# Kernel optimization log

Measured on AMD Instinct MI355X. Metric: run time of the kernel, lower is better.

## Reference

```python
import jax, jax.numpy as jnp
import numpy as np

INPUT_SIZE = 512
SLOT_SIZE = 256
MLP_HIDDEN = 512
NUM_SLOTS = 8
NUM_ITERS = 3
EPSILON = 1e-6
LN_EPS = 1e-5


def _layernorm(x, g, b):
    m = jnp.mean(x, axis=-1, keepdims=True)
    v = jnp.mean(jnp.square(x - m), axis=-1, keepdims=True)
    return (x - m) * jax.lax.rsqrt(v + LN_EPS) * g + b


def setup_inputs() -> dict:
    key = jax.random.key(0)
    ks = jax.random.split(key, 16)
    N, B, W = 32, 64, 24
    s = 0.02
    inp = {
        "sentence": jax.random.normal(ks[0], (N, B, W, INPUT_SIZE), jnp.float32),
        "sentence_sum": jax.random.normal(ks[1], (N, B, INPUT_SIZE), jnp.float32),
        "mask": jax.random.randint(ks[2], (N, B, W), 0, 2, jnp.int32),
        "Wk": jax.random.normal(ks[3], (INPUT_SIZE, SLOT_SIZE), jnp.float32) * s,
        "bk": jnp.zeros((SLOT_SIZE,), jnp.float32),
        "Wv": jax.random.normal(ks[4], (INPUT_SIZE, SLOT_SIZE), jnp.float32) * s,
        "bv": jnp.zeros((SLOT_SIZE,), jnp.float32),
        "Wq": jax.random.normal(ks[5], (SLOT_SIZE, SLOT_SIZE), jnp.float32) * s,
        "bq": jnp.zeros((SLOT_SIZE,), jnp.float32),
        "g_ln": jnp.ones((SLOT_SIZE,), jnp.float32),
        "b_ln": jnp.zeros((SLOT_SIZE,), jnp.float32),
        "W1": jax.random.normal(ks[6], (SLOT_SIZE, MLP_HIDDEN), jnp.float32) * s,
        "b1": jnp.zeros((MLP_HIDDEN,), jnp.float32),
        "W2": jax.random.normal(ks[7], (MLP_HIDDEN, SLOT_SIZE), jnp.float32) * s,
        "b2": jnp.zeros((SLOT_SIZE,), jnp.float32),
        "Wbind": jax.random.normal(ks[8], (INPUT_SIZE, NUM_SLOTS * SLOT_SIZE), jnp.float32) * s,
        "bbind": jnp.zeros((NUM_SLOTS * SLOT_SIZE,), jnp.float32),
        "Wproj": jax.random.normal(ks[9], (2 * SLOT_SIZE, SLOT_SIZE), jnp.float32) * s,
        "bproj": jnp.zeros((SLOT_SIZE,), jnp.float32),
    }
    return inp


def reference(sentence, sentence_sum, mask, Wk, bk, Wv, bv, Wq, bq, g_ln, b_ln,
              W1, b1, W2, b2, Wbind, bbind, Wproj, bproj):
    N, B = sentence.shape[0], sentence.shape[1]
    # initial slots from the sentence summary: [N, B, NUM_SLOTS, SLOT]
    initial_slots = (sentence_sum @ Wbind + bbind).reshape(N, B, NUM_SLOTS, SLOT_SIZE)
    # additive mask on the word axis: [N, B, W, 1]
    maskf = -1e6 * (1.0 - mask.astype(jnp.float32))[..., None]
    # elu(+1) feature maps for keys; plain linear values
    k = jax.nn.elu(sentence @ Wk + bk) + 1.0  # [N,B,W,SLOT]
    v = sentence @ Wv + bv                    # [N,B,W,SLOT]

    scale = 1.0 / SLOT_SIZE
    slots = initial_slots
    for _ in range(NUM_ITERS):
        q = (slots @ Wq + bq) + initial_slots
        q = jax.nn.elu(q * (SLOT_SIZE ** -0.5)) + 1.0  # [N,B,S,SLOT]
        attn_logits = jnp.einsum('nbis,nbjs->nbij', k, q) + maskf  # [N,B,W,S]
        attn = jax.nn.softmax(attn_logits, axis=3) + EPSILON
        attn = attn / jnp.sum(attn, axis=2, keepdims=True)  # renorm over words
        updates = jnp.einsum('nbij,nbik->nbjk', attn, v)    # [N,B,S,SLOT]
        h = _layernorm(updates, g_ln, b_ln)
        h = jax.nn.relu(h @ W1 + b1) @ W2 + b2
        slots = slots + h * scale

    # dropout is identity in eval mode
    slots = jnp.concatenate([initial_slots, slots], axis=-1)
    slots = slots @ Wproj + bproj
    return slots
```

## Files before the change

kernel.cpp:

```cpp
#include <hip/hip_runtime.h>
#include <hip/hip_bf16.h>
#include <math.h>

typedef unsigned int uint;
typedef unsigned short ushort;
typedef __attribute__((ext_vector_type(8))) short bf16x8;
typedef __attribute__((ext_vector_type(4))) float f32x4;

__device__ __forceinline__ float bu2f(ushort u){ union{uint u; float f;} v; v.u = ((uint)u)<<16; return v.f; }
__device__ __forceinline__ ushort f2bu(float x){ union{float f; uint u;} v; v.f = x; uint r = (v.u + 0x7FFFu + ((v.u>>16)&1u))>>16; return (ushort)r; }
__device__ __forceinline__ uint pack2(float a, float b){ return (uint)f2bu(a) | ((uint)f2bu(b) << 16); }
__device__ __forceinline__ uint cvtpk2(float a, float b){
    uint r; asm("v_cvt_pk_bf16_f32 %0, %1, %2" : "=v"(r) : "v"(a), "v"(b)); return r;
}
__device__ __forceinline__ void gload16(const ushort* g, ushort* l){
    __builtin_amdgcn_global_load_lds(
        (const __attribute__((address_space(1))) uint*)g,
        (__attribute__((address_space(3))) uint*)l, 16, 0, 0);
}

#define GEPI_IS0   0
#define GEPI_Q     2
#define GEPI_RELU  3
#define GEPI_MLP2  4
#define GEPI_OUT   5
#define GEPI_MLP2L 6

#define SWZ(r, c) (((r) << 5) + ((((c) ^ ((r) >> 1)) & 3) << 3))


template<int EPI, int CB>
__global__ __launch_bounds__(256) void gemm64(
    const ushort* __restrict__ Abf, int lda,
    const ushort* __restrict__ Bt,
    const float* __restrict__ xb0,
    float* __restrict__ fp0,
    ushort* __restrict__ up0, ushort* __restrict__ up1,
    int M, int N, int K)
{
    __shared__ ushort As[64 * 32];
    __shared__ ushort Bs[64 * 32];
    int tid = threadIdx.x;
    int wave = tid >> 6, lane = tid & 63;
    int wr = wave >> 1, wc = wave & 1;
    int quad = lane >> 4, l15 = lane & 15;

    constexpr int LCB = (CB == 4) ? 2 : (CB == 8) ? 3 : 5;
    int bid = blockIdx.x;
    int x8  = bid & 7;
    int tt  = bid >> 3;
    int cb  = tt & (CB - 1);
    int rb  = ((tt >> LCB) << 3) + x8;
    int row0 = rb * 64, col0 = cb * 64;

    int r   = (wave << 4) + (lane >> 2);
    int csw = ((((lane & 3) ^ (r >> 1)) & 3) << 3);
    ushort* Alds = &As[wave << 9];
    ushort* Blds = &Bs[wave << 9];
    const ushort* Ag = Abf + (size_t)(row0 + r) * lda + csw;
    const ushort* Bg = Bt  + (size_t)(col0 + r) * K   + csw;

    f32x4 acc[2][2];
    #pragma unroll
    for (int i = 0; i < 2; i++)
        #pragma unroll
        for (int j = 0; j < 2; j++) acc[i][j] = (f32x4){0.f, 0.f, 0.f, 0.f};

    for (int k0 = 0; k0 < K; k0 += 32) {
        gload16(Ag + k0, Alds);
        gload16(Bg + k0, Blds);
        __syncthreads();
        bf16x8 af[2], bfr[2];
        #pragma unroll
        for (int mt = 0; mt < 2; mt++) {
            int ar = wr * 32 + mt * 16 + l15;
            af[mt] = *(const bf16x8*)&As[SWZ(ar, quad)];
        }
        #pragma unroll
        for (int nt = 0; nt < 2; nt++) {
            int br = wc * 32 + nt * 16 + l15;
            bfr[nt] = *(const bf16x8*)&Bs[SWZ(br, quad)];
        }
        #pragma unroll
        for (int mt = 0; mt < 2; mt++)
            #pragma unroll
            for (int nt = 0; nt < 2; nt++)
                acc[mt][nt] = __builtin_amdgcn_mfma_f32_16x16x32_bf16(
                    af[mt], bfr[nt], acc[mt][nt], 0, 0, 0);
        __syncthreads();
    }

    #pragma unroll
    for (int mt = 0; mt < 2; mt++) {
        #pragma unroll
        for (int nt = 0; nt < 2; nt++) {
            #pragma unroll
            for (int reg = 0; reg < 4; reg++) {
                int gr = row0 + wr * 32 + mt * 16 + quad * 4 + reg;
                int gc = col0 + wc * 32 + nt * 16 + l15;
                float x = acc[mt][nt][reg] + xb0[gc];
                if (EPI == GEPI_IS0) {
                    size_t srow = (size_t)gr * 8 + (gc >> 8);
                    int dim = gc & 255;
                    fp0[srow * 256 + dim] = x;
                    ushort xb = f2bu(x);
                    up0[srow * 512 + dim]       = xb;
                    up0[srow * 512 + 256 + dim] = xb;
                } else if (EPI == GEPI_Q) {
                    float y = (x + bu2f(up1[(size_t)gr * 512 + gc])) * 0.0625f;
                    y = y > 0.f ? y + 1.f : expf(y);
                    up0[(size_t)gr * 256 + gc] = f2bu(y);
                } else if (EPI == GEPI_RELU) {
                    up0[(size_t)gr * 512 + gc] = f2bu(fmaxf(x, 0.f));
                } else if (EPI == GEPI_MLP2 || EPI == GEPI_MLP2L) {
                    size_t i = (size_t)gr * 256 + gc;
                    float s = fp0[i] + x * (1.f / 256.f);
                    if (EPI == GEPI_MLP2) fp0[i] = s;
                    up0[(size_t)gr * 512 + 256 + gc] = f2bu(s);
                } else {
                    fp0[(size_t)gr * 256 + gc] = x;
                }
            }
        }
    }
}

__global__ __launch_bounds__(256) void gemm_kv64(
    const ushort* __restrict__ A0,
    const ushort* __restrict__ A1,
    const ushort* __restrict__ Bt,
    const float* __restrict__ bk, const float* __restrict__ bv,
    ushort* __restrict__ kbuf, ushort* __restrict__ vbuf, int K)
{
    __shared__ ushort As[64 * 32];
    __shared__ ushort Bs[64 * 32];
    int tid = threadIdx.x;
    int wave = tid >> 6, lane = tid & 63;
    int wr = wave >> 1, wc = wave & 1;
    int quad = lane >> 4, l15 = lane & 15;

    int bid = blockIdx.x;
    int x8  = bid & 7;
    int tt  = bid >> 3;
    int cb  = tt & 7;
    int rb  = (tt >> 3) * 8 + x8;
    int row0 = rb * 64, col0 = cb * 64;

    int r   = (wave << 4) + (lane >> 2);
    int csw = ((((lane & 3) ^ (r >> 1)) & 3) << 3);
    ushort* Alds = &As[wave << 9];
    ushort* Blds = &Bs[wave << 9];
    const ushort* Ag = (row0 < 32768)
        ? (A0 + (size_t)(row0 + r) * K + csw)
        : (A1 + (size_t)(row0 - 32768 + r) * K + csw);
    const ushort* Bg = Bt + (size_t)(col0 + r) * K + csw;

    f32x4 acc[2][2];
    #pragma unroll
    for (int i = 0; i < 2; i++)
        #pragma unroll
        for (int j = 0; j < 2; j++) acc[i][j] = (f32x4){0.f, 0.f, 0.f, 0.f};

    for (int k0 = 0; k0 < K; k0 += 32) {
        gload16(Ag + k0, Alds);
        gload16(Bg + k0, Blds);
        __syncthreads();
        bf16x8 af[2], bfr[2];
        #pragma unroll
        for (int mt = 0; mt < 2; mt++) {
            int ar = wr * 32 + mt * 16 + l15;
            af[mt] = *(const bf16x8*)&As[SWZ(ar, quad)];
        }
        #pragma unroll
        for (int nt = 0; nt < 2; nt++) {
            int br = wc * 32 + nt * 16 + l15;
            bfr[nt] = *(const bf16x8*)&Bs[SWZ(br, quad)];
        }
        #pragma unroll
        for (int mt = 0; mt < 2; mt++)
            #pragma unroll
            for (int nt = 0; nt < 2; nt++)
                acc[mt][nt] = __builtin_amdgcn_mfma_f32_16x16x32_bf16(
                    af[mt], bfr[nt], acc[mt][nt], 0, 0, 0);
        __syncthreads();
    }

    bool isK = (col0 < 256);
    const float* __restrict__ bias = isK ? bk : bv;
    ushort* __restrict__ outp = isK ? kbuf : vbuf;
    int cbase = isK ? col0 : col0 - 256;

    #pragma unroll
    for (int mt = 0; mt < 2; mt++) {
        #pragma unroll
        for (int nt = 0; nt < 2; nt++) {
            #pragma unroll
            for (int reg = 0; reg < 4; reg++) {
                int gr = row0 + wr * 32 + mt * 16 + quad * 4 + reg;
                int gc = cbase + wc * 32 + nt * 16 + l15;
                float x = acc[mt][nt][reg] + bias[gc];
                if (isK) x = x > 0.f ? x + 1.f : expf(x);
                outp[(size_t)gr * 256 + gc] = f2bu(x);
            }
        }
    }
}

__global__ __launch_bounds__(256) void prep_kernel(
    const float* __restrict__ sentence,
    const float* __restrict__ sent_sum,
    const float* __restrict__ Wbind, const float* __restrict__ Wk,
    const float* __restrict__ Wv, const float* __restrict__ Wq,
    const float* __restrict__ W1, const float* __restrict__ W2,
    const float* __restrict__ Wproj,
    ushort* __restrict__ sentA0, ushort* __restrict__ sentA1,
    ushort* __restrict__ ssum_bf,
    ushort* __restrict__ Wbind_t, ushort* __restrict__ Wkv_t,
    ushort* __restrict__ Wq_t, ushort* __restrict__ W1_t,
    ushort* __restrict__ W2_t, ushort* __restrict__ Wproj_t)
{
    int gid = blockIdx.x * 256 + threadIdx.x;
    if (gid < 6291456) {
        float4 f = ((const float4*)sentence)[gid];
        uint2 o; o.x = cvtpk2(f.x, f.y); o.y = cvtpk2(f.z, f.w);
        if (gid < 4194304) ((uint2*)sentA0)[gid] = o;
        else               ((uint2*)sentA1)[gid - 4194304] = o;
        return;
    }
    int idx = gid - 6291456;
    if (idx < 262144) {
        float4 f = ((const float4*)sent_sum)[idx];
        uint2 o; o.x = pack2(f.x, f.y); o.y = pack2(f.z, f.w);
        ((uint2*)ssum_bf)[idx] = o; return;
    }
    idx -= 262144;
    if (idx < 1048576) { int n = idx >> 9, k = idx & 511;
        Wbind_t[idx] = f2bu(Wbind[(size_t)k * 2048 + n]); return; }
    idx -= 1048576;
    if (idx < 262144) { int n = idx >> 9, k = idx & 511;
        Wkv_t[idx] = f2bu(n < 256 ? Wk[(size_t)k * 256 + n] : Wv[(size_t)k * 256 + n - 256]); return; }
    idx -= 262144;
    if (idx < 65536) { int n = idx >> 8, k = idx & 255;
        Wq_t[idx] = f2bu(Wq[(size_t)k * 256 + n]); return; }
    idx -= 65536;
    if (idx < 131072) { int n = idx >> 8, k = idx & 255;
        W1_t[idx] = f2bu(W1[(size_t)k * 512 + n]); return; }
    idx -= 131072;
    if (idx < 131072) { int n = idx >> 9, k = idx & 511;
        W2_t[idx] = f2bu(W2[(size_t)k * 256 + n]); return; }
    idx -= 131072;
    if (idx < 131072) { int n = idx >> 9, k = idx & 511;
        Wproj_t[idx] = f2bu(Wproj[(size_t)k * 256 + n]); return; }
}

__global__ __launch_bounds__(256) void attn_kernel(
    const ushort* __restrict__ kbuf, const ushort* __restrict__ vbuf,
    const ushort* __restrict__ qbuf, const int* __restrict__ mask,
    const float* __restrict__ g_ln, const float* __restrict__ b_ln,
    ushort* __restrict__ ubuf)
{
    const int W = 24, S = 8;
    __shared__ ushort kk[24 * 264], vv[24 * 264], qsb[8 * 264];
    __shared__ float us[8 * 257];
    __shared__ float attnw[24][8];
    __shared__ float colsum[8], mean_s[8], rstd_s[8], maskf[24];

    int nb = blockIdx.x, t = threadIdx.x;
    size_t bw = (size_t)nb * W * 256, bs = (size_t)nb * S * 256;

    for (int l = t; l < 3072; l += 256) {
        int row = l >> 7, col = l & 127;
        ((uint*)kk)[row * 132 + col] = ((const uint*)(kbuf + bw))[l];
        ((uint*)vv)[row * 132 + col] = ((const uint*)(vbuf + bw))[l];
    }
    for (int l = t; l < 1024; l += 256) {
        int row = l >> 7, col = l & 127;
        ((uint*)qsb)[row * 132 + col] = ((const uint*)(qbuf + bs))[l];
    }
    if (t < W) maskf[t] = mask[(size_t)nb * W + t] ? 0.f : -1e6f;
    __syncthreads();

    if (t < W * S) {
        int i = t >> 3, j = t & 7;
        float a = 0.f;
        for (int d0 = 0; d0 < 256; d0 += 8) {
            bf16x8 kv8 = *(const bf16x8*)&kk[i * 264 + d0];
            bf16x8 qv8 = *(const bf16x8*)&qsb[j * 264 + d0];
            #pragma unroll
            for (int m = 0; m < 8; m++)
                a += bu2f((ushort)kv8[m]) * bu2f((ushort)qv8[m]);
        }
        attnw[i][j] = a + maskf[i];
    }
    __syncthreads();

    if (t < W) {
        float m = attnw[t][0];
        #pragma unroll
        for (int j = 1; j < S; j++) m = fmaxf(m, attnw[t][j]);
        float e[S]; float s = 0.f;
        #pragma unroll
        for (int j = 0; j < S; j++) { e[j] = expf(attnw[t][j] - m); s += e[j]; }
        #pragma unroll
        for (int j = 0; j < S; j++) attnw[t][j] = e[j] / s + 1e-6f;
    }
    __syncthreads();

    if (t < S) {
        float s = 0.f;
        for (int i = 0; i < W; i++) s += attnw[i][t];
        colsum[t] = s;
    }
    __syncthreads();

    {
        float acc[S] = {};
        #pragma unroll
        for (int i = 0; i < W; i++) {
            float vx = bu2f(vv[i * 264 + t]);
            float4 w0 = *(const float4*)&attnw[i][0];
            float4 w1 = *(const float4*)&attnw[i][4];
            acc[0] += w0.x * vx; acc[1] += w0.y * vx;
            acc[2] += w0.z * vx; acc[3] += w0.w * vx;
            acc[4] += w1.x * vx; acc[5] += w1.y * vx;
            acc[6] += w1.z * vx; acc[7] += w1.w * vx;
        }
        #pragma unroll
        for (int j = 0; j < S; j++) us[j * 257 + t] = acc[j] / colsum[j];
    }
    __syncthreads();

    {
        int lane = t & 63;
        #pragma unroll
        for (int jj = 0; jj < 2; jj++) {
            int j = (t >> 6) * 2 + jj;
            float x0 = us[j * 257 + lane],       x1 = us[j * 257 + lane + 64];
            float x2 = us[j * 257 + lane + 128], x3 = us[j * 257 + lane + 192];
            float p = x0 + x1 + x2 + x3;
            for (int off = 32; off; off >>= 1) p += __shfl_xor(p, off);
            float mean = p * (1.f / 256.f);
            float d0 = x0 - mean, d1 = x1 - mean, d2 = x2 - mean, d3 = x3 - mean;
            float vr = d0 * d0 + d1 * d1 + d2 * d2 + d3 * d3;
            for (int off = 32; off; off >>= 1) vr += __shfl_xor(vr, off);
            if (lane == 0) {
                mean_s[j] = mean;
                rstd_s[j] = rsqrtf(vr * (1.f / 256.f) + 1e-5f);
            }
        }
    }
    __syncthreads();

    {
        float g = g_ln[t], bb = b_ln[t];
        #pragma unroll
        for (int j = 0; j < S; j++)
            ubuf[bs + j * 256 + t] = f2bu((us[j * 257 + t] - mean_s[j]) * rstd_s[j] * g + bb);
    }
}

__global__ __launch_bounds__(256) void mega_kernel(
    const float* __restrict__ sentence, const float* __restrict__ sent_sum,
    const int*  __restrict__ mask,
    const float* __restrict__ Wk, const float* __restrict__ bk,
    const float* __restrict__ Wv, const float* __restrict__ bv,
    const float* __restrict__ Wq, const float* __restrict__ bq,
    const float* __restrict__ g_ln, const float* __restrict__ b_ln,
    const float* __restrict__ W1, const float* __restrict__ b1,
    const float* __restrict__ W2, const float* __restrict__ b2,
    const float* __restrict__ Wbind, const float* __restrict__ bbind,
    const float* __restrict__ Wproj, const float* __restrict__ bproj,
    float* __restrict__ out)
{
    const int W = 24, S = 8, D = 256, IN = 512, H = 512;
    __shared__ float seh[2048];
    __shared__ ushort kk[24 * 256];
    __shared__ ushort vv[24 * 256];
    __shared__ float is0s[8 * 256];
    __shared__ float sl[8 * 256];
    __shared__ float qv[8 * 256];
    __shared__ float attnw[24][8];
    __shared__ float colsum[8], mean_s[8], rstd_s[8], maskf[24];

    int nb = blockIdx.x, t = threadIdx.x;
    size_t sbase = (size_t)nb * W * IN;

    if (t < W) maskf[t] = mask[(size_t)nb * W + t] ? 0.f : -1e6f;
    for (int l = t; l < IN; l += 256) seh[l] = sent_sum[(size_t)nb * IN + l];
    __syncthreads();
    {
        float acc[S];
        #pragma unroll
        for (int j = 0; j < S; j++) acc[j] = bbind[j * D + t];
        for (int c = 0; c < IN; c++) {
            float sc = seh[c];
            #pragma unroll
            for (int j = 0; j < S; j++) acc[j] += sc * Wbind[(size_t)c * (S * D) + j * D + t];
        }
        #pragma unroll
        for (int j = 0; j < S; j++) { is0s[j * D + t] = acc[j]; sl[j * D + t] = acc[j]; }
    }
    {
        float ka[W], va[W];
        float bkv = bk[t], bvv = bv[t];
        #pragma unroll
        for (int i = 0; i < W; i++) { ka[i] = bkv; va[i] = bvv; }
        for (int ch = 0; ch < 8; ch++) {
            __syncthreads();
            for (int l = t; l < W * 64; l += 256) {
                int i = l >> 6, c = l & 63;
                seh[l] = sentence[sbase + (size_t)i * IN + ch * 64 + c];
            }
            __syncthreads();
            for (int c = 0; c < 64; c++) {
                int cg = ch * 64 + c;
                float wk = Wk[(size_t)cg * D + t];
                float wv = Wv[(size_t)cg * D + t];
                #pragma unroll
                for (int i = 0; i < W; i++) {
                    float s = seh[i * 64 + c];
                    ka[i] += s * wk; va[i] += s * wv;
                }
            }
        }
        #pragma unroll
        for (int i = 0; i < W; i++) {
            float kx = ka[i];
            kk[i * D + t] = f2bu(kx > 0.f ? kx + 1.f : expf(kx));
            vv[i * D + t] = f2bu(va[i]);
        }
    }
    __syncthreads();

    for (int it = 0; it < 3; it++) {
        {
            float qa[S]; float bqv = bq[t];
            #pragma unroll
            for (int j = 0; j < S; j++) qa[j] = bqv + is0s[j * D + t];
            for (int c = 0; c < D; c++) {
                float wq = Wq[(size_t)c * D + t];
                #pragma unroll
                for (int j = 0; j < S; j++) qa[j] += sl[j * D + c] * wq;
            }
            #pragma unroll
            for (int j = 0; j < S; j++) {
                float y = qa[j] * 0.0625f;
                qv[j * D + t] = y > 0.f ? y + 1.f : expf(y);
            }
        }
        __syncthreads();
        if (t < W * S) {
            int i = t >> 3, j = t & 7;
            float a = 0.f;
            #pragma unroll 8
            for (int d = 0; d < D; d++) a += bu2f(kk[i * D + d]) * qv[j * D + d];
            attnw[i][j] = a + maskf[i];
        }
        __syncthreads();
        if (t < W) {
            float m = attnw[t][0];
            #pragma unroll
            for (int j = 1; j < S; j++) m = fmaxf(m, attnw[t][j]);
            float e[S]; float s = 0.f;
            #pragma unroll
            for (int j = 0; j < S; j++) { e[j] = expf(attnw[t][j] - m); s += e[j]; }
            #pragma unroll
            for (int j = 0; j < S; j++) attnw[t][j] = e[j] / s + 1e-6f;
        }
        __syncthreads();
        if (t < S) {
            float s = 0.f;
            for (int i = 0; i < W; i++) s += attnw[i][t];
            colsum[t] = s;
        }
        __syncthreads();
        {
            float acc[S] = {};
            #pragma unroll
            for (int i = 0; i < W; i++) {
                float vx = bu2f(vv[i * D + t]);
                #pragma unroll
                for (int j = 0; j < S; j++) acc[j] += attnw[i][j] * vx;
            }
            #pragma unroll
            for (int j = 0; j < S; j++) qv[j * D + t] = acc[j] / colsum[j];
        }
        __syncthreads();
        {
            int lane = t & 63;
            #pragma unroll
            for (int jj = 0; jj < 2; jj++) {
                int j = (t >> 6) * 2 + jj;
                float x0 = qv[j * D + lane],       x1 = qv[j * D + lane + 64];
                float x2 = qv[j * D + lane + 128], x3 = qv[j * D + lane + 192];
                float p = x0 + x1 + x2 + x3;
                for (int off = 32; off; off >>= 1) p += __shfl_xor(p, off);
                float mean = p * (1.f / 256.f);
                float d0 = x0 - mean, d1 = x1 - mean, d2 = x2 - mean, d3 = x3 - mean;
                float vr = d0 * d0 + d1 * d1 + d2 * d2 + d3 * d3;
                for (int off = 32; off; off >>= 1) vr += __shfl_xor(vr, off);
                if (lane == 0) { mean_s[j] = mean; rstd_s[j] = rsqrtf(vr * (1.f / 256.f) + 1e-5f); }
            }
        }
        __syncthreads();
        {
            float g = g_ln[t], bb = b_ln[t];
            #pragma unroll
            for (int j = 0; j < S; j++)
                qv[j * D + t] = (qv[j * D + t] - mean_s[j]) * rstd_s[j] * g + bb;
        }
        __syncthreads();
        {
            float sa[S]; float b2v = b2[t];
            #pragma unroll
            for (int j = 0; j < S; j++) sa[j] = b2v;
            for (int half = 0; half < 2; half++) {
                int hcol = half * 256 + t;
                float ha[S]; float b1v = b1[hcol];
                #pragma unroll
                for (int j = 0; j < S; j++) ha[j] = b1v;
                for (int d = 0; d < D; d++) {
                    float w1 = W1[(size_t)d * H + hcol];
                    #pragma unroll
                    for (int j = 0; j < S; j++) ha[j] += qv[j * D + d] * w1;
                }
                __syncthreads();
                #pragma unroll
                for (int j = 0; j < S; j++) seh[j * D + t] = fmaxf(ha[j], 0.f);
                __syncthreads();
                for (int h = 0; h < 256; h++) {
                    float w2 = W2[(size_t)(half * 256 + h) * D + t];
                    #pragma unroll
                    for (int j = 0; j < S; j++) sa[j] += seh[j * D + h] * w2;
                }
            }
            __syncthreads();
            #pragma unroll
            for (int j = 0; j < S; j++) sl[j * D + t] += sa[j] * (1.f / 256.f);
        }
        __syncthreads();
    }
    {
        float oa[S]; float bpv = bproj[t];
        #pragma unroll
        for (int j = 0; j < S; j++) oa[j] = bpv;
        for (int c = 0; c < D; c++) {
            float wp1 = Wproj[(size_t)c * D + t];
            float wp2 = Wproj[(size_t)(D + c) * D + t];
            #pragma unroll
            for (int j = 0; j < S; j++)
                oa[j] += is0s[j * D + c] * wp1 + sl[j * D + c] * wp2;
        }
        #pragma unroll
        for (int j = 0; j < S; j++)
            out[(size_t)nb * (S * D) + j * D + t] = oa[j];
    }
}

extern "C" void kernel_launch(void* const* d_in, const int* in_sizes, int n_in,
                              void* d_out, int out_size, void* d_ws, size_t ws_size,
                              hipStream_t stream)
{
    const float* sentence = (const float*)d_in[0];
    const float* sent_sum = (const float*)d_in[1];
    const int*  mask      = (const int*)d_in[2];
    const float* Wk = (const float*)d_in[3];  const float* bk = (const float*)d_in[4];
    const float* Wv = (const float*)d_in[5];  const float* bv = (const float*)d_in[6];
    const float* Wq = (const float*)d_in[7];  const float* bq = (const float*)d_in[8];
    const float* g_ln = (const float*)d_in[9];  const float* b_ln = (const float*)d_in[10];
    const float* W1 = (const float*)d_in[11]; const float* b1 = (const float*)d_in[12];
    const float* W2 = (const float*)d_in[13]; const float* b2 = (const float*)d_in[14];
    const float* Wbind = (const float*)d_in[15]; const float* bbind = (const float*)d_in[16];
    const float* Wproj = (const float*)d_in[17]; const float* bproj = (const float*)d_in[18];
    float* out = (float*)d_out;

    const size_t WS_NEEDED = 123076608ULL;
    if (ws_size >= WS_NEEDED) {
        char* w = (char*)d_ws;
        float*  slots   = (float*) (w);
        ushort* catb    = (ushort*)(w + 16777216);
        ushort* kbuf    = (ushort*)(w + 33554432);
        ushort* vbuf    = (ushort*)(w + 58720256);
        ushort* qbuf    = (ushort*)(w + 83886080);
        ushort* ubuf    = (ushort*)(w + 92274688);
        ushort* hbuf    = (ushort*)(w + 100663296);
        ushort* ssum_bf = (ushort*)(w + 117440512);
        ushort* Wbind_t = (ushort*)(w + 119537664);
        ushort* Wkv_t   = (ushort*)(w + 121634816);
        ushort* Wq_t    = (ushort*)(w + 122159104);
        ushort* W1_t    = (ushort*)(w + 122290176);
        ushort* W2_t    = (ushort*)(w + 122552320);
        ushort* Wproj_t = (ushort*)(w + 122814464);

        ushort* sentA0 = (ushort*)(w);
        ushort* sentA1 = (ushort*)(w + 83886080);

        prep_kernel<<<dim3(32512), dim3(256), 0, stream>>>(
            sentence, sent_sum, Wbind, Wk, Wv, Wq, W1, W2, Wproj,
            sentA0, sentA1,
            ssum_bf, Wbind_t, Wkv_t, Wq_t, W1_t, W2_t, Wproj_t);

        gemm_kv64<<<dim3(6144), dim3(256), 0, stream>>>(
            sentA0, sentA1, Wkv_t, bk, bv, kbuf, vbuf, 512);

        gemm64<GEPI_IS0, 32><<<dim3(1024), dim3(256), 0, stream>>>(
            ssum_bf, 512, Wbind_t, bbind,
            slots, catb, nullptr, 2048, 2048, 512);

        for (int it = 0; it < 3; it++) {
            gemm64<GEPI_Q, 4><<<dim3(1024), dim3(256), 0, stream>>>(
                catb + 256, 512, Wq_t, bq,
                nullptr, qbuf, catb, 16384, 256, 256);
            attn_kernel<<<dim3(2048), dim3(256), 0, stream>>>(
                kbuf, vbuf, qbuf, mask, g_ln, b_ln, ubuf);
            gemm64<GEPI_RELU, 8><<<dim3(2048), dim3(256), 0, stream>>>(
                ubuf, 256, W1_t, b1,
                nullptr, hbuf, nullptr, 16384, 512, 256);
            if (it < 2)
                gemm64<GEPI_MLP2, 4><<<dim3(1024), dim3(256), 0, stream>>>(
                    hbuf, 512, W2_t, b2,
                    slots, catb, nullptr, 16384, 256, 512);
            else
                gemm64<GEPI_MLP2L, 4><<<dim3(1024), dim3(256), 0, stream>>>(
                    hbuf, 512, W2_t, b2,
                    slots, catb, nullptr, 16384, 256, 512);
        }

        gemm64<GEPI_OUT, 4><<<dim3(1024), dim3(256), 0, stream>>>(
            catb, 512, Wproj_t, bproj,
            out, nullptr, nullptr, 16384, 256, 512);
    } else {
        mega_kernel<<<dim3(2048), dim3(256), 0, stream>>>(
            sentence, sent_sum, mask, Wk, bk, Wv, bv, Wq, bq, g_ln, b_ln,
            W1, b1, W2, b2, Wbind, bbind, Wproj, bproj, out);
    }
}
```

Measured before the change: 462.9 us.

## Fuse Q projection GEMM into attention kernel using per-block MFMA

```diff
diff --git a/kernel.cpp b/kernel.cpp
--- a/kernel.cpp
+++ b/kernel.cpp
@@ -20,14 +20,12 @@
 }
 
 #define GEPI_IS0   0
-#define GEPI_Q     2
 #define GEPI_RELU  3
 #define GEPI_MLP2  4
 #define GEPI_OUT   5
 #define GEPI_MLP2L 6
 
 #define SWZ(r, c) (((r) << 5) + ((((c) ^ ((r) >> 1)) & 3) << 3))
-
 
 template<int EPI, int CB>
 __global__ __launch_bounds__(256) void gemm64(
@@ -106,10 +104,6 @@
                     ushort xb = f2bu(x);
                     up0[srow * 512 + dim]       = xb;
                     up0[srow * 512 + 256 + dim] = xb;
-                } else if (EPI == GEPI_Q) {
-                    float y = (x + bu2f(up1[(size_t)gr * 512 + gc])) * 0.0625f;
-                    y = y > 0.f ? y + 1.f : expf(y);
-                    up0[(size_t)gr * 256 + gc] = f2bu(y);
                 } else if (EPI == GEPI_RELU) {
                     up0[(size_t)gr * 512 + gc] = f2bu(fmaxf(x, 0.f));
                 } else if (EPI == GEPI_MLP2 || EPI == GEPI_MLP2L) {
@@ -255,29 +249,69 @@
 
 __global__ __launch_bounds__(256) void attn_kernel(
     const ushort* __restrict__ kbuf, const ushort* __restrict__ vbuf,
-    const ushort* __restrict__ qbuf, const int* __restrict__ mask,
+    const ushort* __restrict__ catb,
+    const ushort* __restrict__ Wqt,
+    const float*  __restrict__ bq,
+    const int* __restrict__ mask,
     const float* __restrict__ g_ln, const float* __restrict__ b_ln,
     ushort* __restrict__ ubuf)
 {
     const int W = 24, S = 8;
-    __shared__ ushort kk[24 * 264], vv[24 * 264], qsb[8 * 264];
-    __shared__ float us[8 * 257];
+    __shared__ ushort kk[24 * 264], qsb[8 * 264];
+    __shared__ __align__(16) float us[8 * 257];
     __shared__ float attnw[24][8];
     __shared__ float colsum[8], mean_s[8], rstd_s[8], maskf[24];
+    ushort* uQ = (ushort*)us;
 
     int nb = blockIdx.x, t = threadIdx.x;
+    int wave = t >> 6, lane = t & 63;
+    int quad = lane >> 4, l15 = lane & 15;
     size_t bw = (size_t)nb * W * 256, bs = (size_t)nb * S * 256;
 
     for (int l = t; l < 3072; l += 256) {
         int row = l >> 7, col = l & 127;
         ((uint*)kk)[row * 132 + col] = ((const uint*)(kbuf + bw))[l];
-        ((uint*)vv)[row * 132 + col] = ((const uint*)(vbuf + bw))[l];
-    }
-    for (int l = t; l < 1024; l += 256) {
-        int row = l >> 7, col = l & 127;
-        ((uint*)qsb)[row * 132 + col] = ((const uint*)(qbuf + bs))[l];
+    }
+    {
+        int r = t >> 4, cc = t & 15;
+        uint4 v = (uint4){0u, 0u, 0u, 0u};
+        if (r < 8) v = *(const uint4*)(catb + (size_t)(nb * 8 + r) * 512 + 256 + cc * 8);
+        *(uint4*)&uQ[(cc >> 2) * 512 + SWZ(r, cc & 3)] = v;
     }
     if (t < W) maskf[t] = mask[(size_t)nb * W + t] ? 0.f : -1e6f;
+    __syncthreads();
+
+    {
+        f32x4 qa[4];
+        #pragma unroll
+        for (int i = 0; i < 4; i++) qa[i] = (f32x4){0.f, 0.f, 0.f, 0.f};
+        #pragma unroll
+        for (int kc = 0; kc < 8; kc++) {
+            bf16x8 a = *(const bf16x8*)&uQ[kc * 512 + SWZ(l15, quad)];
+            #pragma unroll
+            for (int ct = 0; ct < 4; ct++) {
+                int n = wave * 64 + ct * 16 + l15;
+                bf16x8 b = *(const bf16x8*)(Wqt + (size_t)n * 256 + kc * 32 + quad * 8);
+                qa[ct] = __builtin_amdgcn_mfma_f32_16x16x32_bf16(a, b, qa[ct], 0, 0, 0);
+            }
+        }
+        __syncthreads();
+        #pragma unroll
+        for (int ct = 0; ct < 4; ct++) {
+            int col = wave * 64 + ct * 16 + l15;
+            #pragma unroll
+            for (int reg = 0; reg < 4; reg++) {
+                int row = quad * 4 + reg;
+                if (row < 8) {
+                    float x = qa[ct][reg] + bq[col]
+                            + bu2f(catb[(size_t)(nb * 8 + row) * 512 + col]);
+                    float y = x * 0.0625f;
+                    y = y > 0.f ? y + 1.f : expf(y);
+                    qsb[row * 264 + col] = f2bu(y);
+                }
+            }
+        }
+    }
     __syncthreads();
 
     if (t < W * S) {
@@ -317,7 +351,7 @@
         float acc[S] = {};
         #pragma unroll
         for (int i = 0; i < W; i++) {
-            float vx = bu2f(vv[i * 264 + t]);
+            float vx = bu2f(vbuf[bw + (size_t)i * 256 + t]);
             float4 w0 = *(const float4*)&attnw[i][0];
             float4 w1 = *(const float4*)&attnw[i][4];
             acc[0] += w0.x * vx; acc[1] += w0.y * vx;
@@ -331,19 +365,19 @@
     __syncthreads();
 
     {
-        int lane = t & 63;
+        int l63 = t & 63;
         #pragma unroll
         for (int jj = 0; jj < 2; jj++) {
             int j = (t >> 6) * 2 + jj;
-            float x0 = us[j * 257 + lane],       x1 = us[j * 257 + lane + 64];
-            float x2 = us[j * 257 + lane + 128], x3 = us[j * 257 + lane + 192];
+            float x0 = us[j * 257 + l63],       x1 = us[j * 257 + l63 + 64];
+            float x2 = us[j * 257 + l63 + 128], x3 = us[j * 257 + l63 + 192];
             float p = x0 + x1 + x2 + x3;
             for (int off = 32; off; off >>= 1) p += __shfl_xor(p, off);
             float mean = p * (1.f / 256.f);
             float d0 = x0 - mean, d1 = x1 - mean, d2 = x2 - mean, d3 = x3 - mean;
             float vr = d0 * d0 + d1 * d1 + d2 * d2 + d3 * d3;
             for (int off = 32; off; off >>= 1) vr += __shfl_xor(vr, off);
-            if (lane == 0) {
+            if (l63 == 0) {
                 mean_s[j] = mean;
                 rstd_s[j] = rsqrtf(vr * (1.f / 256.f) + 1e-5f);
             }
@@ -581,7 +615,6 @@
         ushort* catb    = (ushort*)(w + 16777216);
         ushort* kbuf    = (ushort*)(w + 33554432);
         ushort* vbuf    = (ushort*)(w + 58720256);
-        ushort* qbuf    = (ushort*)(w + 83886080);
         ushort* ubuf    = (ushort*)(w + 92274688);
         ushort* hbuf    = (ushort*)(w + 100663296);
         ushort* ssum_bf = (ushort*)(w + 117440512);
@@ -608,11 +641,8 @@
             slots, catb, nullptr, 2048, 2048, 512);
 
         for (int it = 0; it < 3; it++) {
-            gemm64<GEPI_Q, 4><<<dim3(1024), dim3(256), 0, stream>>>(
-                catb + 256, 512, Wq_t, bq,
-                nullptr, qbuf, catb, 16384, 256, 256);
             attn_kernel<<<dim3(2048), dim3(256), 0, stream>>>(
-                kbuf, vbuf, qbuf, mask, g_ln, b_ln, ubuf);
+                kbuf, vbuf, catb, Wq_t, bq, mask, g_ln, b_ln, ubuf);
             gemm64<GEPI_RELU, 8><<<dim3(2048), dim3(256), 0, stream>>>(
                 ubuf, 256, W1_t, b1,
                 nullptr, hbuf, nullptr, 16384, 512, 256);
```

Result: slower. 523.7 us (+13.1%).

## Load two K-slices per barrier in GEMMs and read V directly in attention

Applied to the files above, without the earlier changes.

```diff
diff --git a/kernel.cpp b/kernel.cpp
--- a/kernel.cpp
+++ b/kernel.cpp
@@ -27,7 +27,6 @@
 #define GEPI_MLP2L 6
 
 #define SWZ(r, c) (((r) << 5) + ((((c) ^ ((r) >> 1)) & 3) << 3))
-
 
 template<int EPI, int CB>
 __global__ __launch_bounds__(256) void gemm64(
@@ -38,8 +37,8 @@
     ushort* __restrict__ up0, ushort* __restrict__ up1,
     int M, int N, int K)
 {
-    __shared__ ushort As[64 * 32];
-    __shared__ ushort Bs[64 * 32];
+    __shared__ ushort As[2][64 * 32];
+    __shared__ ushort Bs[2][64 * 32];
     int tid = threadIdx.x;
     int wave = tid >> 6, lane = tid & 63;
     int wr = wave >> 1, wc = wave & 1;
@@ -55,8 +54,6 @@
 
     int r   = (wave << 4) + (lane >> 2);
     int csw = ((((lane & 3) ^ (r >> 1)) & 3) << 3);
-    ushort* Alds = &As[wave << 9];
-    ushort* Blds = &Bs[wave << 9];
     const ushort* Ag = Abf + (size_t)(row0 + r) * lda + csw;
     const ushort* Bg = Bt  + (size_t)(col0 + r) * K   + csw;
 
@@ -66,27 +63,32 @@
         #pragma unroll
         for (int j = 0; j < 2; j++) acc[i][j] = (f32x4){0.f, 0.f, 0.f, 0.f};
 
-    for (int k0 = 0; k0 < K; k0 += 32) {
-        gload16(Ag + k0, Alds);
-        gload16(Bg + k0, Blds);
-        __syncthreads();
-        bf16x8 af[2], bfr[2];
-        #pragma unroll
-        for (int mt = 0; mt < 2; mt++) {
-            int ar = wr * 32 + mt * 16 + l15;
-            af[mt] = *(const bf16x8*)&As[SWZ(ar, quad)];
-        }
-        #pragma unroll
-        for (int nt = 0; nt < 2; nt++) {
-            int br = wc * 32 + nt * 16 + l15;
-            bfr[nt] = *(const bf16x8*)&Bs[SWZ(br, quad)];
-        }
-        #pragma unroll
-        for (int mt = 0; mt < 2; mt++)
-            #pragma unroll
-            for (int nt = 0; nt < 2; nt++)
-                acc[mt][nt] = __builtin_amdgcn_mfma_f32_16x16x32_bf16(
-                    af[mt], bfr[nt], acc[mt][nt], 0, 0, 0);
+    for (int k0 = 0; k0 < K; k0 += 64) {
+        gload16(Ag + k0,      &As[0][wave << 9]);
+        gload16(Bg + k0,      &Bs[0][wave << 9]);
+        gload16(Ag + k0 + 32, &As[1][wave << 9]);
+        gload16(Bg + k0 + 32, &Bs[1][wave << 9]);
+        __syncthreads();
+        #pragma unroll
+        for (int b = 0; b < 2; b++) {
+            bf16x8 af[2], bfr[2];
+            #pragma unroll
+            for (int mt = 0; mt < 2; mt++) {
+                int ar = wr * 32 + mt * 16 + l15;
+                af[mt] = *(const bf16x8*)&As[b][SWZ(ar, quad)];
+            }
+            #pragma unroll
+            for (int nt = 0; nt < 2; nt++) {
+                int br = wc * 32 + nt * 16 + l15;
+                bfr[nt] = *(const bf16x8*)&Bs[b][SWZ(br, quad)];
+            }
+            #pragma unroll
+            for (int mt = 0; mt < 2; mt++)
+                #pragma unroll
+                for (int nt = 0; nt < 2; nt++)
+                    acc[mt][nt] = __builtin_amdgcn_mfma_f32_16x16x32_bf16(
+                        af[mt], bfr[nt], acc[mt][nt], 0, 0, 0);
+        }
         __syncthreads();
     }
 
@@ -132,8 +134,8 @@
     const float* __restrict__ bk, const float* __restrict__ bv,
     ushort* __restrict__ kbuf, ushort* __restrict__ vbuf, int K)
 {
-    __shared__ ushort As[64 * 32];
-    __shared__ ushort Bs[64 * 32];
+    __shared__ ushort As[2][64 * 32];
+    __shared__ ushort Bs[2][64 * 32];
     int tid = threadIdx.x;
     int wave = tid >> 6, lane = tid & 63;
     int wr = wave >> 1, wc = wave & 1;
@@ -148,8 +150,6 @@
 
     int r   = (wave << 4) + (lane >> 2);
     int csw = ((((lane & 3) ^ (r >> 1)) & 3) << 3);
-    ushort* Alds = &As[wave << 9];
-    ushort* Blds = &Bs[wave << 9];
     const ushort* Ag = (row0 < 32768)
         ? (A0 + (size_t)(row0 + r) * K + csw)
         : (A1 + (size_t)(row0 - 32768 + r) * K + csw);
@@ -161,27 +161,32 @@
         #pragma unroll
         for (int j = 0; j < 2; j++) acc[i][j] = (f32x4){0.f, 0.f, 0.f, 0.f};
 
-    for (int k0 = 0; k0 < K; k0 += 32) {
-        gload16(Ag + k0, Alds);
-        gload16(Bg + k0, Blds);
-        __syncthreads();
-        bf16x8 af[2], bfr[2];
-        #pragma unroll
-        for (int mt = 0; mt < 2; mt++) {
-            int ar = wr * 32 + mt * 16 + l15;
-            af[mt] = *(const bf16x8*)&As[SWZ(ar, quad)];
-        }
-        #pragma unroll
-        for (int nt = 0; nt < 2; nt++) {
-            int br = wc * 32 + nt * 16 + l15;
-            bfr[nt] = *(const bf16x8*)&Bs[SWZ(br, quad)];
-        }
-        #pragma unroll
-        for (int mt = 0; mt < 2; mt++)
-            #pragma unroll
-            for (int nt = 0; nt < 2; nt++)
-                acc[mt][nt] = __builtin_amdgcn_mfma_f32_16x16x32_bf16(
-                    af[mt], bfr[nt], acc[mt][nt], 0, 0, 0);
+    for (int k0 = 0; k0 < K; k0 += 64) {
+        gload16(Ag + k0,      &As[0][wave << 9]);
+        gload16(Bg + k0,      &Bs[0][wave << 9]);
+        gload16(Ag + k0 + 32, &As[1][wave << 9]);
+        gload16(Bg + k0 + 32, &Bs[1][wave << 9]);
+        __syncthreads();
+        #pragma unroll
+        for (int b = 0; b < 2; b++) {
+            bf16x8 af[2], bfr[2];
+            #pragma unroll
+            for (int mt = 0; mt < 2; mt++) {
+                int ar = wr * 32 + mt * 16 + l15;
+                af[mt] = *(const bf16x8*)&As[b][SWZ(ar, quad)];
+            }
+            #pragma unroll
+            for (int nt = 0; nt < 2; nt++) {
+                int br = wc * 32 + nt * 16 + l15;
+                bfr[nt] = *(const bf16x8*)&Bs[b][SWZ(br, quad)];
+            }
+            #pragma unroll
+            for (int mt = 0; mt < 2; mt++)
+                #pragma unroll
+                for (int nt = 0; nt < 2; nt++)
+                    acc[mt][nt] = __builtin_amdgcn_mfma_f32_16x16x32_bf16(
+                        af[mt], bfr[nt], acc[mt][nt], 0, 0, 0);
+        }
         __syncthreads();
     }
 
@@ -260,7 +265,7 @@
     ushort* __restrict__ ubuf)
 {
     const int W = 24, S = 8;
-    __shared__ ushort kk[24 * 264], vv[24 * 264], qsb[8 * 264];
+    __shared__ ushort kk[24 * 264], qsb[8 * 264];
     __shared__ float us[8 * 257];
     __shared__ float attnw[24][8];
     __shared__ float colsum[8], mean_s[8], rstd_s[8], maskf[24];
@@ -271,7 +276,6 @@
     for (int l = t; l < 3072; l += 256) {
         int row = l >> 7, col = l & 127;
         ((uint*)kk)[row * 132 + col] = ((const uint*)(kbuf + bw))[l];
-        ((uint*)vv)[row * 132 + col] = ((const uint*)(vbuf + bw))[l];
     }
     for (int l = t; l < 1024; l += 256) {
         int row = l >> 7, col = l & 127;
@@ -317,7 +321,7 @@
         float acc[S] = {};
         #pragma unroll
         for (int i = 0; i < W; i++) {
-            float vx = bu2f(vv[i * 264 + t]);
+            float vx = bu2f(vbuf[bw + (size_t)i * 256 + t]);
             float4 w0 = *(const float4*)&attnw[i][0];
             float4 w1 = *(const float4*)&attnw[i][4];
             acc[0] += w0.x * vx; acc[1] += w0.y * vx;
```

After: 433.3 us. 1.07x faster.
